# Performance work log

Measured on AMD Instinct MI355X. Metric: run time of the kernel, lower is better.

Reference implementation:

```python
import jax, jax.numpy as jnp
import numpy as np

EPS = 1e-06

def _feature_map(x):
    # elu_feature_map: phi(x) = elu(x) + 1  (strictly positive features)
    return jax.nn.elu(x) + 1.0

def setup_inputs() -> dict:
    key = jax.random.key(0)
    kq, kk, kv = jax.random.split(key, 3)
    N, L, H, D, M = 2, 2048, 8, 64, 64
    return {
        "queries": jax.random.normal(kq, (N, L, H, D), dtype=jnp.float32),
        "keys": jax.random.normal(kk, (N, L, H, D), dtype=jnp.float32),
        "values": jax.random.normal(kv, (N, L, H, M), dtype=jnp.float32),
    }

def reference(queries, keys, values):
    Q = _feature_map(queries)   # [N,L,H,D]
    K = _feature_map(keys)      # [N,L,H,D]
    # normalizer: Z_i = 1 / (Q_i . sum_{j<=i} K_j + eps)
    Z = 1.0 / (jnp.einsum('nlhi,nlhi->nlh', Q, jnp.cumsum(K, axis=1)) + EPS)
    # causal linear attention: S_i = sum_{j<=i} K_j outer V_j ; out_i = Q_i @ S_i
    S = jnp.cumsum(jnp.einsum('nlhd,nlhm->nlhdm', K, values), axis=1)  # [N,L,H,D,M]
    V = jnp.einsum('nlhd,nlhdm->nlhm', Q, S)
    return V * Z[:, :, :, None]
```

## Files before the change

kernel.cpp:

```cpp
#include <hip/hip_runtime.h>


namespace {
constexpr int N_ = 2, L_ = 2048, H_ = 8, D_ = 64, M_ = 64;
constexpr int C  = 64;
constexpr int G  = L_ / C;
constexpr int NH = N_ * H_;
constexpr int LDH = H_ * D_;
constexpr int TS  = 72;
constexpr float EPS_ = 1e-6f;
}

typedef __attribute__((ext_vector_type(8))) short short8;
typedef __attribute__((ext_vector_type(4))) float f32x4;

__device__ __forceinline__ float phi(float x) {
    return x > 0.0f ? x + 1.0f : __expf(x);
}
__device__ __forceinline__ unsigned short f2bf(float x) {
    unsigned int u = __float_as_uint(x);
    u += 0x7fffu + ((u >> 16) & 1u);
    return (unsigned short)(u >> 16);
}
__device__ __forceinline__ float bf2f(unsigned short h) {
    return __uint_as_float(((unsigned int)h) << 16);
}
__device__ __forceinline__ ushort4 pack4(float a, float b, float c, float d) {
    ushort4 p; p.x = f2bf(a); p.y = f2bf(b); p.z = f2bf(c); p.w = f2bf(d);
    return p;
}

__global__ __launch_bounds__(256, 4) void k_chunksum(
    const float* __restrict__ keys, const float* __restrict__ values,
    unsigned short* __restrict__ wsSb, float* __restrict__ wsK)
{
    __shared__ __align__(16) unsigned short Kt[C * TS];
    __shared__ __align__(16) unsigned short Vt[C * TS];
    const int bid = blockIdx.x;
    const int g = bid % G, nh = bid / G;
    const int n = nh / H_, h = nh % H_;
    const int t = threadIdx.x;
    const size_t base = ((size_t)(n * L_ + g * C) * H_ + h) * D_;

#pragma unroll
    for (int r = 0; r < 4; ++r) {
        const int f = t + 256 * r;
        const int j = f >> 4, c = (f & 15) * 4;
        const size_t ga = base + (size_t)j * LDH + c;
        const float4 kv = *(const float4*)(keys + ga);
        const float4 vv = *(const float4*)(values + ga);
        Kt[(c + 0) * TS + j] = f2bf(phi(kv.x));
        Kt[(c + 1) * TS + j] = f2bf(phi(kv.y));
        Kt[(c + 2) * TS + j] = f2bf(phi(kv.z));
        Kt[(c + 3) * TS + j] = f2bf(phi(kv.w));
        Vt[(c + 0) * TS + j] = f2bf(vv.x);
        Vt[(c + 1) * TS + j] = f2bf(vv.y);
        Vt[(c + 2) * TS + j] = f2bf(vv.z);
        Vt[(c + 3) * TS + j] = f2bf(vv.w);
    }
    __syncthreads();

    const int w = t >> 6, lane = t & 63;
    const int row16 = lane & 15, quad = lane >> 4;

    f32x4 acc[4] = {f32x4{0,0,0,0}, f32x4{0,0,0,0}, f32x4{0,0,0,0}, f32x4{0,0,0,0}};
    f32x4 accK = f32x4{0,0,0,0};
    short8 ones;
#pragma unroll
    for (int i = 0; i < 8; ++i) ones[i] = (short)0x3F80;

#pragma unroll
    for (int kt = 0; kt < 2; ++kt) {
        const short8 a = *(const short8*)&Kt[(16 * w + row16) * TS + quad * 8 + 32 * kt];
#pragma unroll
        for (int c = 0; c < 4; ++c) {
            const short8 b = *(const short8*)&Vt[(16 * c + row16) * TS + quad * 8 + 32 * kt];
            acc[c] = __builtin_amdgcn_mfma_f32_16x16x32_bf16(a, b, acc[c], 0, 0, 0);
        }
        accK = __builtin_amdgcn_mfma_f32_16x16x32_bf16(a, ones, accK, 0, 0, 0);
    }

    unsigned short* Sc = wsSb + (size_t)bid * (D_ * M_);
#pragma unroll
    for (int c = 0; c < 4; ++c) {
        *(ushort4*)(Sc + (16 * c + row16) * D_ + 16 * w + quad * 4) =
            pack4(acc[c][0], acc[c][1], acc[c][2], acc[c][3]);
    }

    if (row16 == 0) {
#pragma unroll
        for (int r = 0; r < 4; ++r)
            wsK[(size_t)bid * D_ + 16 * w + quad * 4 + r] = accK[r];
    }
}

__global__ __launch_bounds__(128) void k_scan(
    unsigned short* __restrict__ wsSb, float* __restrict__ wsK)
{
    const int bid = blockIdx.x;
    const int nh = bid >> 4, q = bid & 15;
    const int t = threadIdx.x;

    unsigned int* base =
        (unsigned int*)(wsSb + (size_t)nh * G * (D_ * M_) + q * 256 + t * 2);
    float r0 = 0.f, r1 = 0.f;
#pragma unroll
    for (int g = 0; g < G; ++g) {
        unsigned int* p = base + (size_t)g * (D_ * M_ / 2);
        const unsigned int v = *p;
        const float v0 = bf2f((unsigned short)(v & 0xffffu));
        const float v1 = bf2f((unsigned short)(v >> 16));
        *p = ((unsigned int)f2bf(r1) << 16) | (unsigned int)f2bf(r0);
        r0 += v0; r1 += v1;
    }

    if (q == 0 && t < D_) {
        float rk = 0.f;
        float* kb = wsK + (size_t)nh * G * D_ + t;
#pragma unroll
        for (int g = 0; g < G; ++g) {
            float* p = kb + (size_t)g * D_;
            const float v = *p;
            *p = rk;
            rk += v;
        }
    }
}

__global__ __launch_bounds__(256, 4) void k_out(
    const float* __restrict__ queries, const float* __restrict__ keys,
    const float* __restrict__ values, float* __restrict__ out,
    const unsigned short* __restrict__ wsSb, const float* __restrict__ wsK)
{
    __shared__ __align__(16) unsigned short Qb[C * TS];
    __shared__ __align__(16) unsigned short Kb[C * TS];
    __shared__ __align__(16) unsigned short Vt[C * TS];
    __shared__ __align__(16) unsigned short St[C * TS];

    const int bid = blockIdx.x;
    const int g = bid % G, nh = bid / G;
    const int n = nh / H_, h = nh % H_;
    const int t = threadIdx.x;
    const size_t base = ((size_t)(n * L_ + g * C) * H_ + h) * D_;
    const unsigned short* Spb = wsSb + (size_t)bid * (D_ * M_);
    const float* kpref = wsK + (size_t)bid * D_;

#pragma unroll
    for (int r = 0; r < 4; ++r) {
        const int f = t + 256 * r;
        const int row = f >> 4, c = (f & 15) * 4;
        const size_t ga = base + (size_t)row * LDH + c;
        const float4 qv = *(const float4*)(queries + ga);
        const float4 kv = *(const float4*)(keys + ga);
        const float4 vv = *(const float4*)(values + ga);
        *(ushort4*)&Qb[row * TS + c] = pack4(phi(qv.x), phi(qv.y), phi(qv.z), phi(qv.w));
        *(ushort4*)&Kb[row * TS + c] = pack4(phi(kv.x), phi(kv.y), phi(kv.z), phi(kv.w));
        Vt[(c + 0) * TS + row] = f2bf(vv.x);
        Vt[(c + 1) * TS + row] = f2bf(vv.y);
        Vt[(c + 2) * TS + row] = f2bf(vv.z);
        Vt[(c + 3) * TS + row] = f2bf(vv.w);
    }
#pragma unroll
    for (int r = 0; r < 2; ++r) {
        const int idx = t + 256 * r;
        const int m = idx >> 3, dg = (idx & 7) * 8;
        *(short8*)&St[m * TS + dg] = *(const short8*)(Spb + m * D_ + dg);
    }

    const int w = t >> 6, lane = t & 63;
    const int row16 = lane & 15, quad = lane >> 4;

    const float* kp0 = kpref + quad * 8;
    const float4 kfa = *(const float4*)(kp0);
    const float4 kfb = *(const float4*)(kp0 + 4);
    const float4 kfc = *(const float4*)(kp0 + 32);
    const float4 kfd = *(const float4*)(kp0 + 36);
    short8 bZhi0, bZhi1, bZlo0, bZlo1;
    {
        const float f0[8] = {kfa.x, kfa.y, kfa.z, kfa.w, kfb.x, kfb.y, kfb.z, kfb.w};
        const float f1[8] = {kfc.x, kfc.y, kfc.z, kfc.w, kfd.x, kfd.y, kfd.z, kfd.w};
#pragma unroll
        for (int i = 0; i < 8; ++i) {
            const unsigned short h0 = f2bf(f0[i]);
            bZhi0[i] = (short)h0;
            bZlo0[i] = (short)f2bf(f0[i] - bf2f(h0));
            const unsigned short h1 = f2bf(f1[i]);
            bZhi1[i] = (short)h1;
            bZlo1[i] = (short)f2bf(f1[i] - bf2f(h1));
        }
    }
    __syncthreads();

    short8 aq[2];
#pragma unroll
    for (int kt = 0; kt < 2; ++kt)
        aq[kt] = *(const short8*)&Qb[(16 * w + row16) * TS + quad * 8 + 32 * kt];

    f32x4 accA[4] = {f32x4{0,0,0,0}, f32x4{0,0,0,0}, f32x4{0,0,0,0}, f32x4{0,0,0,0}};
#pragma unroll
    for (int kt = 0; kt < 2; ++kt)
#pragma unroll
        for (int c = 0; c < 4; ++c) {
            const short8 b = *(const short8*)&Kb[(16 * c + row16) * TS + quad * 8 + 32 * kt];
            accA[c] = __builtin_amdgcn_mfma_f32_16x16x32_bf16(aq[kt], b, accA[c], 0, 0, 0);
        }

    f32x4 accZ = f32x4{0, 0, 0, 0};
    accZ = __builtin_amdgcn_mfma_f32_16x16x32_bf16(aq[0], bZhi0, accZ, 0, 0, 0);
    accZ = __builtin_amdgcn_mfma_f32_16x16x32_bf16(aq[1], bZhi1, accZ, 0, 0, 0);
    accZ = __builtin_amdgcn_mfma_f32_16x16x32_bf16(aq[0], bZlo0, accZ, 0, 0, 0);
    accZ = __builtin_amdgcn_mfma_f32_16x16x32_bf16(aq[1], bZlo1, accZ, 0, 0, 0);

    float rs[4] = {0.f, 0.f, 0.f, 0.f};
#pragma unroll
    for (int c = 0; c < 4; ++c)
#pragma unroll
        for (int r = 0; r < 4; ++r) {
            const int row = 16 * w + quad * 4 + r;
            const int col = 16 * c + row16;
            const float v = (col <= row) ? accA[c][r] : 0.f;
            accA[c][r] = v;
            rs[r] += v;
        }
#pragma unroll
    for (int off = 1; off < 16; off <<= 1)
#pragma unroll
        for (int r = 0; r < 4; ++r)
            rs[r] += __shfl_xor(rs[r], off, 64);

    __syncthreads();

#pragma unroll
    for (int c = 0; c < 4; ++c)
#pragma unroll
        for (int r = 0; r < 4; ++r)
            Kb[(16 * w + quad * 4 + r) * TS + 16 * c + row16] = f2bf(accA[c][r]);

    f32x4 accO[4] = {f32x4{0,0,0,0}, f32x4{0,0,0,0}, f32x4{0,0,0,0}, f32x4{0,0,0,0}};
#pragma unroll
    for (int kt = 0; kt < 2; ++kt) {
        const short8 aA = *(const short8*)&Kb[(16 * w + row16) * TS + quad * 8 + 32 * kt];
#pragma unroll
        for (int c = 0; c < 4; ++c) {
            const short8 bV = *(const short8*)&Vt[(16 * c + row16) * TS + quad * 8 + 32 * kt];
            accO[c] = __builtin_amdgcn_mfma_f32_16x16x32_bf16(aA, bV, accO[c], 0, 0, 0);
        }
#pragma unroll
        for (int c = 0; c < 4; ++c) {
            const short8 bS = *(const short8*)&St[(16 * c + row16) * TS + quad * 8 + 32 * kt];
            accO[c] = __builtin_amdgcn_mfma_f32_16x16x32_bf16(aq[kt], bS, accO[c], 0, 0, 0);
        }
    }

#pragma unroll
    for (int r = 0; r < 4; ++r) {
        const int row = 16 * w + quad * 4 + r;
        const float z = 1.0f / (accZ[r] + rs[r] + EPS_);
        const size_t ob = ((size_t)(n * L_ + g * C + row) * H_ + h) * M_;
#pragma unroll
        for (int c = 0; c < 4; ++c)
            out[ob + 16 * c + row16] = accO[c][r] * z;
    }
}

extern "C" void kernel_launch(void* const* d_in, const int* in_sizes, int n_in,
                              void* d_out, int out_size, void* d_ws, size_t ws_size,
                              hipStream_t stream) {
    const float* q = (const float*)d_in[0];
    const float* k = (const float*)d_in[1];
    const float* v = (const float*)d_in[2];
    float* out = (float*)d_out;
    unsigned short* wsSb = (unsigned short*)d_ws;
    float* wsK = (float*)((char*)d_ws + (size_t)NH * G * D_ * M_ * 2);

    k_chunksum<<<dim3(NH * G), dim3(256), 0, stream>>>(k, v, wsSb, wsK);
    k_scan<<<dim3(NH * 16), dim3(128), 0, stream>>>(wsSb, wsK);
    k_out<<<dim3(NH * G), dim3(256), 0, stream>>>(q, k, v, out, wsSb, wsK);
}
```

Before: 84.92 us.

## Fuse chunksum, scan and output kernels into one persistent kernel with grid barriers

Replaces the three launches (chunk sums, cross-chunk prefix scan, output) with a single kernel of 512 blocks that synchronizes through a software grid barrier built on a global atomic counter. Q, K and V are loaded and converted once into shared memory and reused for both the chunk-sum and output phases, so the second global read of K and V goes away. The scan is spread over all blocks, 64 threads each. The intent is to remove launch gaps and redundant loads. In exchange it relies on all blocks being co-resident (launch_bounds lowered to 2 blocks per CU, more LDS per block), otherwise the barrier deadlocks, and it adds barrier spin overhead.

New measurement: 266.7 us. 3.14x slower.

```diff
diff --git a/kernel.cpp b/kernel.cpp
--- a/kernel.cpp
+++ b/kernel.cpp
@@ -8,6 +8,7 @@
 constexpr int NH = N_ * H_;
 constexpr int LDH = H_ * D_;
 constexpr int TS  = 72;
+constexpr int NBLK = NH * G;
 constexpr float EPS_ = 1e-6f;
 }
 
@@ -30,12 +31,33 @@
     return p;
 }
 
-__global__ __launch_bounds__(256, 4) void k_chunksum(
-    const float* __restrict__ keys, const float* __restrict__ values,
+__device__ unsigned int g_bar = 0;
+
+__device__ __forceinline__ void grid_barrier() {
+    __threadfence();
+    __syncthreads();
+    if (threadIdx.x == 0) {
+        const unsigned ticket = atomicAdd(&g_bar, 1u);
+        const unsigned target = (ticket & ~(unsigned)(NBLK - 1)) + (unsigned)NBLK;
+        while (__hip_atomic_load(&g_bar, __ATOMIC_RELAXED,
+                                 __HIP_MEMORY_SCOPE_AGENT) < target)
+            __builtin_amdgcn_s_sleep(2);
+    }
+    __syncthreads();
+    __threadfence();
+}
+
+__global__ __launch_bounds__(256, 2) void k_fused(
+    const float* __restrict__ queries, const float* __restrict__ keys,
+    const float* __restrict__ values, float* __restrict__ out,
     unsigned short* __restrict__ wsSb, float* __restrict__ wsK)
 {
     __shared__ __align__(16) unsigned short Kt[C * TS];
     __shared__ __align__(16) unsigned short Vt[C * TS];
+    __shared__ __align__(16) unsigned short Qb[C * TS];
+    __shared__ __align__(16) unsigned short Kb[C * TS];
+    __shared__ __align__(16) unsigned short St[C * TS];
+
     const int bid = blockIdx.x;
     const int g = bid % G, nh = bid / G;
     const int n = nh / H_, h = nh % H_;
@@ -49,10 +71,16 @@
         const size_t ga = base + (size_t)j * LDH + c;
         const float4 kv = *(const float4*)(keys + ga);
         const float4 vv = *(const float4*)(values + ga);
-        Kt[(c + 0) * TS + j] = f2bf(phi(kv.x));
-        Kt[(c + 1) * TS + j] = f2bf(phi(kv.y));
-        Kt[(c + 2) * TS + j] = f2bf(phi(kv.z));
-        Kt[(c + 3) * TS + j] = f2bf(phi(kv.w));
+        const float4 qv = *(const float4*)(queries + ga);
+        const unsigned short b0 = f2bf(phi(kv.x)), b1 = f2bf(phi(kv.y));
+        const unsigned short b2 = f2bf(phi(kv.z)), b3 = f2bf(phi(kv.w));
+        Kt[(c + 0) * TS + j] = b0;
+        Kt[(c + 1) * TS + j] = b1;
+        Kt[(c + 2) * TS + j] = b2;
+        Kt[(c + 3) * TS + j] = b3;
+        ushort4 pk; pk.x = b0; pk.y = b1; pk.z = b2; pk.w = b3;
+        *(ushort4*)&Kb[j * TS + c] = pk;
+        *(ushort4*)&Qb[j * TS + c] = pack4(phi(qv.x), phi(qv.y), phi(qv.z), phi(qv.w));
         Vt[(c + 0) * TS + j] = f2bf(vv.x);
         Vt[(c + 1) * TS + j] = f2bf(vv.y);
         Vt[(c + 2) * TS + j] = f2bf(vv.z);
@@ -63,112 +91,77 @@
     const int w = t >> 6, lane = t & 63;
     const int row16 = lane & 15, quad = lane >> 4;
 
-    f32x4 acc[4] = {f32x4{0,0,0,0}, f32x4{0,0,0,0}, f32x4{0,0,0,0}, f32x4{0,0,0,0}};
-    f32x4 accK = f32x4{0,0,0,0};
-    short8 ones;
-#pragma unroll
-    for (int i = 0; i < 8; ++i) ones[i] = (short)0x3F80;
-
-#pragma unroll
-    for (int kt = 0; kt < 2; ++kt) {
-        const short8 a = *(const short8*)&Kt[(16 * w + row16) * TS + quad * 8 + 32 * kt];
-#pragma unroll
-        for (int c = 0; c < 4; ++c) {
-            const short8 b = *(const short8*)&Vt[(16 * c + row16) * TS + quad * 8 + 32 * kt];
-            acc[c] = __builtin_amdgcn_mfma_f32_16x16x32_bf16(a, b, acc[c], 0, 0, 0);
-        }
-        accK = __builtin_amdgcn_mfma_f32_16x16x32_bf16(a, ones, accK, 0, 0, 0);
-    }
-
-    unsigned short* Sc = wsSb + (size_t)bid * (D_ * M_);
-#pragma unroll
-    for (int c = 0; c < 4; ++c) {
-        *(ushort4*)(Sc + (16 * c + row16) * D_ + 16 * w + quad * 4) =
-            pack4(acc[c][0], acc[c][1], acc[c][2], acc[c][3]);
-    }
-
-    if (row16 == 0) {
-#pragma unroll
-        for (int r = 0; r < 4; ++r)
-            wsK[(size_t)bid * D_ + 16 * w + quad * 4 + r] = accK[r];
-    }
-}
-
-__global__ __launch_bounds__(128) void k_scan(
-    unsigned short* __restrict__ wsSb, float* __restrict__ wsK)
-{
-    const int bid = blockIdx.x;
-    const int nh = bid >> 4, q = bid & 15;
-    const int t = threadIdx.x;
-
-    unsigned int* base =
-        (unsigned int*)(wsSb + (size_t)nh * G * (D_ * M_) + q * 256 + t * 2);
-    float r0 = 0.f, r1 = 0.f;
-#pragma unroll
-    for (int g = 0; g < G; ++g) {
-        unsigned int* p = base + (size_t)g * (D_ * M_ / 2);
-        const unsigned int v = *p;
-        const float v0 = bf2f((unsigned short)(v & 0xffffu));
-        const float v1 = bf2f((unsigned short)(v >> 16));
-        *p = ((unsigned int)f2bf(r1) << 16) | (unsigned int)f2bf(r0);
-        r0 += v0; r1 += v1;
-    }
-
-    if (q == 0 && t < D_) {
+    {
+        f32x4 acc[4] = {f32x4{0,0,0,0}, f32x4{0,0,0,0}, f32x4{0,0,0,0}, f32x4{0,0,0,0}};
+        f32x4 accK = f32x4{0,0,0,0};
+        short8 ones;
+#pragma unroll
+        for (int i = 0; i < 8; ++i) ones[i] = (short)0x3F80;
+
+#pragma unroll
+        for (int kt = 0; kt < 2; ++kt) {
+            const short8 a = *(const short8*)&Kt[(16 * w + row16) * TS + quad * 8 + 32 * kt];
+#pragma unroll
+            for (int c = 0; c < 4; ++c) {
+                const short8 b = *(const short8*)&Vt[(16 * c + row16) * TS + quad * 8 + 32 * kt];
+                acc[c] = __builtin_amdgcn_mfma_f32_16x16x32_bf16(a, b, acc[c], 0, 0, 0);
+            }
+            accK = __builtin_amdgcn_mfma_f32_16x16x32_bf16(a, ones, accK, 0, 0, 0);
+        }
+
+        unsigned short* Sc = wsSb + (size_t)bid * (D_ * M_);
+#pragma unroll
+        for (int c = 0; c < 4; ++c) {
+            *(ushort4*)(Sc + (16 * c + row16) * D_ + 16 * w + quad * 4) =
+                pack4(acc[c][0], acc[c][1], acc[c][2], acc[c][3]);
+        }
+        if (row16 == 0) {
+#pragma unroll
+            for (int r = 0; r < 4; ++r)
+                wsK[(size_t)bid * D_ + 16 * w + quad * 4 + r] = accK[r];
+        }
+    }
+
+    grid_barrier();
+
+    if (t < 64) {
+        const int cid = bid * 64 + t;
+        const int snh = cid >> 11;
+        const int off = cid & 2047;
+        unsigned int* basep = (unsigned int*)wsSb + (size_t)snh * (G * D_ * M_ / 2) + off;
+        float r0 = 0.f, r1 = 0.f;
+#pragma unroll
+        for (int gg = 0; gg < G; ++gg) {
+            unsigned int* p = basep + (size_t)gg * (D_ * M_ / 2);
+            const unsigned int v = *p;
+            const float v0 = bf2f((unsigned short)(v & 0xffffu));
+            const float v1 = bf2f((unsigned short)(v >> 16));
+            *p = ((unsigned int)f2bf(r1) << 16) | (unsigned int)f2bf(r0);
+            r0 += v0; r1 += v1;
+        }
+    } else if (bid < NH && t < 128) {
+        const int d = t - 64;
         float rk = 0.f;
-        float* kb = wsK + (size_t)nh * G * D_ + t;
-#pragma unroll
-        for (int g = 0; g < G; ++g) {
-            float* p = kb + (size_t)g * D_;
+        float* kb = wsK + (size_t)bid * (G * D_) + d;
+#pragma unroll
+        for (int gg = 0; gg < G; ++gg) {
+            float* p = kb + (size_t)gg * D_;
             const float v = *p;
             *p = rk;
             rk += v;
         }
     }
-}
-
-__global__ __launch_bounds__(256, 4) void k_out(
-    const float* __restrict__ queries, const float* __restrict__ keys,
-    const float* __restrict__ values, float* __restrict__ out,
-    const unsigned short* __restrict__ wsSb, const float* __restrict__ wsK)
-{
-    __shared__ __align__(16) unsigned short Qb[C * TS];
-    __shared__ __align__(16) unsigned short Kb[C * TS];
-    __shared__ __align__(16) unsigned short Vt[C * TS];
-    __shared__ __align__(16) unsigned short St[C * TS];
-
-    const int bid = blockIdx.x;
-    const int g = bid % G, nh = bid / G;
-    const int n = nh / H_, h = nh % H_;
-    const int t = threadIdx.x;
-    const size_t base = ((size_t)(n * L_ + g * C) * H_ + h) * D_;
+
+    grid_barrier();
+
     const unsigned short* Spb = wsSb + (size_t)bid * (D_ * M_);
     const float* kpref = wsK + (size_t)bid * D_;
 
-#pragma unroll
-    for (int r = 0; r < 4; ++r) {
-        const int f = t + 256 * r;
-        const int row = f >> 4, c = (f & 15) * 4;
-        const size_t ga = base + (size_t)row * LDH + c;
-        const float4 qv = *(const float4*)(queries + ga);
-        const float4 kv = *(const float4*)(keys + ga);
-        const float4 vv = *(const float4*)(values + ga);
-        *(ushort4*)&Qb[row * TS + c] = pack4(phi(qv.x), phi(qv.y), phi(qv.z), phi(qv.w));
-        *(ushort4*)&Kb[row * TS + c] = pack4(phi(kv.x), phi(kv.y), phi(kv.z), phi(kv.w));
-        Vt[(c + 0) * TS + row] = f2bf(vv.x);
-        Vt[(c + 1) * TS + row] = f2bf(vv.y);
-        Vt[(c + 2) * TS + row] = f2bf(vv.z);
-        Vt[(c + 3) * TS + row] = f2bf(vv.w);
-    }
-#pragma unroll
-    for (int r = 0; r < 2; ++r) {
-        const int idx = t + 256 * r;
-        const int m = idx >> 3, dg = (idx & 7) * 8;
-        *(short8*)&St[m * TS + dg] = *(const short8*)(Spb + m * D_ + dg);
-    }
-
-    const int w = t >> 6, lane = t & 63;
-    const int row16 = lane & 15, quad = lane >> 4;
+    const int m0 = t >> 3, dg0 = (t & 7) * 8;
+    const int i1 = t + 256;
+    const int m1 = i1 >> 3, dg1 = (i1 & 7) * 8;
+    const short8 s0 = *(const short8*)(Spb + m0 * D_ + dg0);
+    const short8 s1 = *(const short8*)(Spb + m1 * D_ + dg1);
 
     const float* kp0 = kpref + quad * 8;
     const float4 kfa = *(const float4*)(kp0);
@@ -189,7 +182,6 @@
             bZlo1[i] = (short)f2bf(f1[i] - bf2f(h1));
         }
     }
-    __syncthreads();
 
     short8 aq[2];
 #pragma unroll
@@ -235,6 +227,10 @@
 #pragma unroll
         for (int r = 0; r < 4; ++r)
             Kb[(16 * w + quad * 4 + r) * TS + 16 * c + row16] = f2bf(accA[c][r]);
+
+    *(short8*)&St[m0 * TS + dg0] = s0;
+    *(short8*)&St[m1 * TS + dg1] = s1;
+    __syncthreads();
 
     f32x4 accO[4] = {f32x4{0,0,0,0}, f32x4{0,0,0,0}, f32x4{0,0,0,0}, f32x4{0,0,0,0}};
 #pragma unroll
@@ -273,7 +269,5 @@
     unsigned short* wsSb = (unsigned short*)d_ws;
     float* wsK = (float*)((char*)d_ws + (size_t)NH * G * D_ * M_ * 2);
 
-    k_chunksum<<<dim3(NH * G), dim3(256), 0, stream>>>(k, v, wsSb, wsK);
-    k_scan<<<dim3(NH * 16), dim3(128), 0, stream>>>(wsSb, wsK);
-    k_out<<<dim3(NH * G), dim3(256), 0, stream>>>(q, k, v, out, wsSb, wsK);
-}
+    k_fused<<<dim3(NBLK), dim3(256), 0, stream>>>(q, k, v, out, wsSb, wsK);
+}
```
